# Performance work log

Measured on AMD Instinct MI355X. Metric: run time of the kernel, lower is better.

Reference implementation:

```python
import jax, jax.numpy as jnp
import numpy as np

HIDDEN = 64
NUM_LAYERS = 3
EPS = 1e-5


def setup_inputs() -> dict:
    key = jax.random.key(0)
    ks = jax.random.split(key, 16)
    N, E, F_IN, H, C = 100000, 3200000, 12, HIDDEN, 2
    x = jax.random.normal(ks[0], (N, F_IN), dtype=jnp.float32)
    edge_index = jax.random.randint(ks[1], (2, E), 0, N, dtype=jnp.int64)
    s = lambda k, sh, fan: jax.random.normal(k, sh, dtype=jnp.float32) / np.sqrt(fan)
    return {
        "x": x,
        "edge_index": edge_index,
        "W_in": s(ks[2], (F_IN, H), F_IN),
        "b_in": jnp.zeros((H,), jnp.float32),
        "W_g": s(ks[3], (NUM_LAYERS, H, H), H),
        "b_g": jnp.zeros((NUM_LAYERS, H), jnp.float32),
        "gamma": jnp.ones((NUM_LAYERS, H), jnp.float32),
        "beta": jnp.zeros((NUM_LAYERS, H), jnp.float32),
        "W_c1": s(ks[4], (H, H // 2), H),
        "b_c1": jnp.zeros((H // 2,), jnp.float32),
        "W_c2": s(ks[5], (H // 2, C), H // 2),
        "b_c2": jnp.zeros((C,), jnp.float32),
    }


def _gcn_norm(edge_index, N):
    # GCNConv default: add self loops, symmetric normalization D^-1/2 (A+I) D^-1/2
    src, dst = edge_index[0], edge_index[1]
    deg = jax.ops.segment_sum(jnp.ones_like(dst, jnp.float32), dst, num_segments=N) + 1.0
    dinv = jax.lax.rsqrt(deg)
    norm_e = dinv[src] * dinv[dst]          # [E] per-edge coefficient
    self_norm = dinv * dinv                 # [N] self-loop coefficient
    return src, dst, norm_e, self_norm


def _gcn_layer(h, W, b, src, dst, norm_e, self_norm, N):
    h = h @ W                                # [N, H] linear transform first
    agg = jax.ops.segment_sum(h[src] * norm_e[:, None], dst, num_segments=N)
    return agg + h * self_norm[:, None] + b


def _batchnorm(h, gamma, beta):
    mu = jnp.mean(h, axis=0)
    var = jnp.mean(jnp.square(h - mu), axis=0)  # biased, as torch BN
    return (h - mu) * jax.lax.rsqrt(var + EPS) * gamma + beta


def reference(x, edge_index, W_in, b_in, W_g, b_g, gamma, beta, W_c1, b_c1, W_c2, b_c2):
    N = x.shape[0]
    src, dst, norm_e, self_norm = _gcn_norm(edge_index, N)
    h = jax.nn.relu(x @ W_in + b_in)
    for i in range(NUM_LAYERS):
        h = _gcn_layer(h, W_g[i], b_g[i], src, dst, norm_e, self_norm, N)
        h = _batchnorm(h, gamma[i], beta[i])
        if i < NUM_LAYERS - 1:
            h = jax.nn.relu(h)  # dropout omitted (inference/deterministic)
    h = jax.nn.relu(h @ W_c1 + b_c1)
    return h @ W_c2 + b_c2
```

## Files before the change

### kernel.cpp

```cpp
#include <hip/hip_runtime.h>

#define EPSV 1e-5f
#define BSH 8
#define BSZ 256
#define SBR 416

__device__ inline float blo(unsigned u) { return __uint_as_float(u << 16); }
__device__ inline float bhi(unsigned u) { return __uint_as_float(u & 0xFFFF0000u); }
__device__ inline unsigned rne16(float v) {
    unsigned u = __float_as_uint(v);
    return (u + 0x7FFFu + ((u >> 16) & 1u)) >> 16;
}
__device__ inline unsigned pk(float lo, float hi) {
    return (rne16(hi) << 16) | rne16(lo);
}


__global__ __launch_bounds__(256) void k_hist(const int* __restrict__ dst,
                                              int* __restrict__ bcount, int E) {
    __shared__ int hist[1024];
    int t = threadIdx.x;
#pragma unroll
    for (int i = 0; i < 4; i++) hist[t + 256 * i] = 0;
    __syncthreads();
    int e0 = blockIdx.x * 4096;
#pragma unroll
    for (int r = 0; r < 16; r++) {
        int e = e0 + r * 256 + t;
        if (e < E) atomicAdd(&hist[dst[e] >> BSH], 1);
    }
    __syncthreads();
#pragma unroll
    for (int i = 0; i < 4; i++) {
        int bk = t + 256 * i;
        int h = hist[bk];
        if (h) atomicAdd(&bcount[bk], h);
    }
}

__global__ __launch_bounds__(256) void k_bscan(const int* __restrict__ bcount,
                                               int* __restrict__ bstart,
                                               int* __restrict__ gcur, int NB) {
    int t = threadIdx.x;
    int base = t * 4;
    int c[4], s = 0;
#pragma unroll
    for (int i = 0; i < 4; i++) {
        c[i] = (base + i < NB) ? bcount[base + i] : 0;
        s += c[i];
    }
    __shared__ int ls[256];
    ls[t] = s;
    __syncthreads();
    for (int off = 1; off < 256; off <<= 1) {
        int x = (t >= off) ? ls[t - off] : 0;
        __syncthreads();
        ls[t] += x;
        __syncthreads();
    }
    int run = (t == 0) ? 0 : ls[t - 1];
#pragma unroll
    for (int i = 0; i < 4; i++) {
        bstart[base + i] = run;
        gcur[base + i] = run;
        run += c[i];
    }
    if (t == 255) bstart[1024] = ls[255];
}

__global__ __launch_bounds__(256) void k_split(const int* __restrict__ src,
                                               const int* __restrict__ dst,
                                               int* __restrict__ gcur,
                                               unsigned* __restrict__ pairs, int E) {
    __shared__ int hist[1024];
    __shared__ int gb[1024];
    int t = threadIdx.x;
    int e0 = blockIdx.x * 4096;
    int sreg[16], dreg[16];
#pragma unroll
    for (int i = 0; i < 4; i++) hist[t + 256 * i] = 0;
    __syncthreads();
#pragma unroll
    for (int r = 0; r < 16; r++) {
        int e = e0 + r * 256 + t;
        if (e < E) {
            sreg[r] = src[e];
            dreg[r] = dst[e];
            atomicAdd(&hist[dreg[r] >> BSH], 1);
        } else {
            dreg[r] = -1;
        }
    }
    __syncthreads();
#pragma unroll
    for (int i = 0; i < 4; i++) {
        int bk = t + 256 * i;
        int h = hist[bk];
        gb[bk] = h ? atomicAdd(&gcur[bk], h) : 0;
    }
    __syncthreads();
#pragma unroll
    for (int i = 0; i < 4; i++) hist[t + 256 * i] = 0;
    __syncthreads();
#pragma unroll
    for (int r = 0; r < 16; r++) {
        if (dreg[r] >= 0) {
            int bk = dreg[r] >> BSH;
            int rk = atomicAdd(&hist[bk], 1);
            pairs[gb[bk] + rk] = ((unsigned)(dreg[r] & (BSZ - 1)) << 22) |
                                 (unsigned)sreg[r];
        }
    }
}

__global__ __launch_bounds__(256) void k_build(const unsigned* __restrict__ pairs,
                                               const int* __restrict__ bstart,
                                               int* __restrict__ rowptr,
                                               int* __restrict__ rowend,
                                               float* __restrict__ dinv,
                                               int* __restrict__ colidx, int N) {
    int bid = blockIdx.x, t = threadIdx.x;
    int n0 = bid << BSH;
    int e0 = bstart[bid], e1 = bstart[bid + 1];
    __shared__ int cnt[256];
    __shared__ int ls[256];
    __shared__ int cur[256];
    cnt[t] = 0;
    __syncthreads();
    for (int e = e0 + t; e < e1; e += 256)
        atomicAdd(&cnt[pairs[e] >> 22], 1);
    __syncthreads();
    ls[t] = cnt[t];
    __syncthreads();
    for (int off = 1; off < 256; off <<= 1) {
        int x = (t >= off) ? ls[t - off] : 0;
        __syncthreads();
        ls[t] += x;
        __syncthreads();
    }
    int start = e0 + ((t == 0) ? 0 : ls[t - 1]);
    cur[t] = start;
    int node = n0 + t;
    if (node < N) {
        rowptr[node] = start;
        rowend[node] = start + cnt[t];
        dinv[node] = rsqrtf((float)cnt[t] + 1.0f);
    }
    __syncthreads();
    for (int e = e0 + t; e < e1; e += 256) {
        unsigned p = pairs[e];
        int r = atomicAdd(&cur[p >> 22], 1);
        colidx[r] = (int)(p & 0x3FFFFFu);
    }
}


__global__ __launch_bounds__(256) void k_gemm0(const float* __restrict__ x,
                                               const float* __restrict__ Win,
                                               const float* __restrict__ bin,
                                               const float* __restrict__ W,
                                               const float* __restrict__ dinv,
                                               unsigned short* __restrict__ hl, int N) {
    __shared__ float zbuf[4][64];
    int wv = threadIdx.x >> 6;
    int j = threadIdx.x & 63;
    float w[64];
#pragma unroll
    for (int k = 0; k < 64; k++) w[k] = W[k * 64 + j];
    float wi[12];
#pragma unroll
    for (int k = 0; k < 12; k++) wi[k] = Win[k * 64 + j];
    float bj = bin[j];
    const float4* zr = (const float4*)&zbuf[wv][0];
    int wave = (blockIdx.x * 256 + threadIdx.x) >> 6;
    int nw = (gridDim.x * 256) >> 6;
    int node = wave;
    float xa[12];
    if (node < N) {
        const float* xr = x + (size_t)node * 12;
#pragma unroll
        for (int k = 0; k < 12; k++) xa[k] = xr[k];
    }
    for (; node < N; node += nw) {
        int nxt = node + nw;
        float xb[12];
        const float* xr2 = x + (size_t)(nxt < N ? nxt : node) * 12;
#pragma unroll
        for (int k = 0; k < 12; k++) xb[k] = xr2[k];
        float z = bj;
#pragma unroll
        for (int k = 0; k < 12; k++) z = fmaf(xa[k], wi[k], z);
        zbuf[wv][j] = fmaxf(z, 0.0f);
        asm volatile("s_waitcnt lgkmcnt(0)" ::: "memory");
        float acc = 0.0f;
#pragma unroll
        for (int kk = 0; kk < 16; kk++) {
            float4 z4 = zr[kk];
            acc = fmaf(z4.x, w[4 * kk + 0], acc);
            acc = fmaf(z4.y, w[4 * kk + 1], acc);
            acc = fmaf(z4.z, w[4 * kk + 2], acc);
            acc = fmaf(z4.w, w[4 * kk + 3], acc);
        }
        hl[(size_t)node * 64 + j] = (unsigned short)rne16(acc * dinv[node]);
#pragma unroll
        for (int k = 0; k < 12; k++) xa[k] = xb[k];
    }
}

__global__ __launch_bounds__(256) void k_gemmn(const float* __restrict__ W,
                                               const float* __restrict__ ab,
                                               const float* __restrict__ dinv,
                                               const unsigned* __restrict__ h2,
                                               unsigned short* __restrict__ hl, int N) {
    __shared__ float zbuf[4][64];
    int wv = threadIdx.x >> 6;
    int j = threadIdx.x & 63;
    float w[64];
#pragma unroll
    for (int k = 0; k < 64; k++) w[k] = W[k * 64 + j];
    float Aj = ab[j], Bj = ab[64 + j];
    const float4* zr = (const float4*)&zbuf[wv][0];
    int wave = (blockIdx.x * 256 + threadIdx.x) >> 6;
    int nw = (gridDim.x * 256) >> 6;
    int node = wave;
    unsigned u = (node < N) ? h2[(size_t)node * 32 + (j >> 1)] : 0u;
    for (; node < N; node += nw) {
        int nxt = node + nw;
        unsigned unext = h2[(size_t)(nxt < N ? nxt : node) * 32 + (j >> 1)];
        float h = (j & 1) ? bhi(u) : blo(u);
        zbuf[wv][j] = fmaxf(fmaf(Aj, h, Bj), 0.0f);
        asm volatile("s_waitcnt lgkmcnt(0)" ::: "memory");
        float acc = 0.0f;
#pragma unroll
        for (int kk = 0; kk < 16; kk++) {
            float4 z4 = zr[kk];
            acc = fmaf(z4.x, w[4 * kk + 0], acc);
            acc = fmaf(z4.y, w[4 * kk + 1], acc);
            acc = fmaf(z4.z, w[4 * kk + 2], acc);
            acc = fmaf(z4.w, w[4 * kk + 3], acc);
        }
        hl[(size_t)node * 64 + j] = (unsigned short)rne16(acc * dinv[node]);
        u = unext;
    }
}

__global__ __launch_bounds__(256) void k_agg(const int* __restrict__ rowptr,
                                             const int* __restrict__ rowend,
                                             const int* __restrict__ colidx,
                                             const float* __restrict__ dinv,
                                             const unsigned* __restrict__ hl2,
                                             const float* __restrict__ b,
                                             unsigned* __restrict__ out2, int N) {
    int t = threadIdx.x;
    int hw = t >> 5;
    int lane = t & 31;
    int sub = lane >> 3;
    int q = lane & 7;
    int d = blockIdx.x * 8 + hw;
    if (d >= N) return;
    int e0 = rowptr[d], e1 = rowend[d];
    const uint4* H = (const uint4*)hl2;

    float a0 = 0.f, a1 = 0.f, a2 = 0.f, a3 = 0.f;
    float a4 = 0.f, a5 = 0.f, a6 = 0.f, a7 = 0.f;
    float c0 = 0.f, c1 = 0.f, c2 = 0.f, c3 = 0.f;
    float c4 = 0.f, c5 = 0.f, c6 = 0.f, c7 = 0.f;

    if (sub == 0) {
        uint4 su = H[d * 8 + q];
        a0 = blo(su.x); a1 = bhi(su.x);
        a2 = blo(su.y); a3 = bhi(su.y);
        a4 = blo(su.z); a5 = bhi(su.z);
        a6 = blo(su.w); a7 = bhi(su.w);
    }

    int e = e0 + sub;
    for (; e + 12 < e1; e += 16) {
        int s0 = colidx[e];
        int s1 = colidx[e + 4];
        int s2 = colidx[e + 8];
        int s3 = colidx[e + 12];
        uint4 u0 = H[s0 * 8 + q];
        uint4 u1 = H[s1 * 8 + q];
        uint4 u2 = H[s2 * 8 + q];
        uint4 u3 = H[s3 * 8 + q];
        a0 += blo(u0.x); a1 += bhi(u0.x); a2 += blo(u0.y); a3 += bhi(u0.y);
        a4 += blo(u0.z); a5 += bhi(u0.z); a6 += blo(u0.w); a7 += bhi(u0.w);
        c0 += blo(u1.x); c1 += bhi(u1.x); c2 += blo(u1.y); c3 += bhi(u1.y);
        c4 += blo(u1.z); c5 += bhi(u1.z); c6 += blo(u1.w); c7 += bhi(u1.w);
        a0 += blo(u2.x); a1 += bhi(u2.x); a2 += blo(u2.y); a3 += bhi(u2.y);
        a4 += blo(u2.z); a5 += bhi(u2.z); a6 += blo(u2.w); a7 += bhi(u2.w);
        c0 += blo(u3.x); c1 += bhi(u3.x); c2 += blo(u3.y); c3 += bhi(u3.y);
        c4 += blo(u3.z); c5 += bhi(u3.z); c6 += blo(u3.w); c7 += bhi(u3.w);
    }
    for (; e < e1; e += 4) {
        uint4 u = H[colidx[e] * 8 + q];
        a0 += blo(u.x); a1 += bhi(u.x); a2 += blo(u.y); a3 += bhi(u.y);
        a4 += blo(u.z); a5 += bhi(u.z); a6 += blo(u.w); a7 += bhi(u.w);
    }
    a0 += c0; a1 += c1; a2 += c2; a3 += c3;
    a4 += c4; a5 += c5; a6 += c6; a7 += c7;

    a0 += __shfl_xor(a0, 8);  a0 += __shfl_xor(a0, 16);
    a1 += __shfl_xor(a1, 8);  a1 += __shfl_xor(a1, 16);
    a2 += __shfl_xor(a2, 8);  a2 += __shfl_xor(a2, 16);
    a3 += __shfl_xor(a3, 8);  a3 += __shfl_xor(a3, 16);
    a4 += __shfl_xor(a4, 8);  a4 += __shfl_xor(a4, 16);
    a5 += __shfl_xor(a5, 8);  a5 += __shfl_xor(a5, 16);
    a6 += __shfl_xor(a6, 8);  a6 += __shfl_xor(a6, 16);
    a7 += __shfl_xor(a7, 8);  a7 += __shfl_xor(a7, 16);

    if (sub == 0) {
        float dv = dinv[d];
        int fb = q * 8;
        float o0 = fmaf(a0, dv, b[fb + 0]);
        float o1 = fmaf(a1, dv, b[fb + 1]);
        float o2 = fmaf(a2, dv, b[fb + 2]);
        float o3 = fmaf(a3, dv, b[fb + 3]);
        float o4 = fmaf(a4, dv, b[fb + 4]);
        float o5 = fmaf(a5, dv, b[fb + 5]);
        float o6 = fmaf(a6, dv, b[fb + 6]);
        float o7 = fmaf(a7, dv, b[fb + 7]);
        uint4 o;
        o.x = pk(o0, o1);
        o.y = pk(o2, o3);
        o.z = pk(o4, o5);
        o.w = pk(o6, o7);
        ((uint4*)out2)[d * 8 + q] = o;
    }
}

__global__ __launch_bounds__(256) void k_statsred(const unsigned* __restrict__ h2,
                                                  float* __restrict__ ps,
                                                  int* __restrict__ ticket,
                                                  const float* __restrict__ gamma,
                                                  const float* __restrict__ beta,
                                                  float* __restrict__ ab,
                                                  int N, float invN) {
    int t = threadIdx.x;
    int hw = t >> 5, f = t & 31;
    float s0 = 0.f, s1 = 0.f, q0 = 0.f, q1 = 0.f;
    int stride = gridDim.x << 3;
    int n = blockIdx.x * 8 + hw;
    for (; n + 3 * stride < N; n += stride << 2) {
        unsigned ua = h2[(size_t)n * 32 + f];
        unsigned ub = h2[((size_t)n + stride) * 32 + f];
        unsigned uc = h2[((size_t)n + 2 * stride) * 32 + f];
        unsigned ud = h2[((size_t)n + 3 * stride) * 32 + f];
        float r;
        r = blo(ua); s0 += r; q0 = fmaf(r, r, q0);
        r = bhi(ua); s1 += r; q1 = fmaf(r, r, q1);
        r = blo(ub); s0 += r; q0 = fmaf(r, r, q0);
        r = bhi(ub); s1 += r; q1 = fmaf(r, r, q1);
        r = blo(uc); s0 += r; q0 = fmaf(r, r, q0);
        r = bhi(uc); s1 += r; q1 = fmaf(r, r, q1);
        r = blo(ud); s0 += r; q0 = fmaf(r, r, q0);
        r = bhi(ud); s1 += r; q1 = fmaf(r, r, q1);
    }
    for (; n < N; n += stride) {
        unsigned u = h2[(size_t)n * 32 + f];
        float r;
        r = blo(u); s0 += r; q0 = fmaf(r, r, q0);
        r = bhi(u); s1 += r; q1 = fmaf(r, r, q1);
    }
    __shared__ float rs[8][64];
    __shared__ float rq[8][64];
    __shared__ int lastflag;
    rs[hw][2 * f] = s0; rs[hw][2 * f + 1] = s1;
    rq[hw][2 * f] = q0; rq[hw][2 * f + 1] = q1;
    __syncthreads();
    if (t < 128) {
        float acc = 0.f;
#pragma unroll
        for (int h = 0; h < 8; h++) acc += (t < 64) ? rs[h][t] : rq[h][t - 64];
        atomicAdd(&ps[t], acc);
    }
    __syncthreads();
    if (t == 0) {
        __threadfence();
        lastflag = (atomicAdd(ticket, 1) == (int)gridDim.x - 1);
    }
    __syncthreads();
    if (lastflag && t < 64) {
        float S = atomicAdd(&ps[t], 0.0f);
        float Q = atomicAdd(&ps[64 + t], 0.0f);
        float mu = S * invN;
        float var = fmaf(-mu, mu, Q * invN);
        float A = rsqrtf(var + EPSV) * gamma[t];
        ab[t] = A;
        ab[64 + t] = fmaf(-mu, A, beta[t]);
    }
}

__global__ __launch_bounds__(256, 2) void k_cls(const unsigned* __restrict__ h2,
                                                const float* __restrict__ ab,
                                                const float* __restrict__ W1,
                                                const float* __restrict__ b1,
                                                const float* __restrict__ W2,
                                                const float* __restrict__ b2,
                                                float* __restrict__ out, int N) {
    int lane = threadIdx.x & 63;
    int half = lane >> 5, jj = lane & 31;
    float w[64];
    float bj = b1[jj];
#pragma unroll
    for (int k = 0; k < 64; k++) {
        float w1 = W1[k * 32 + jj];
        w[k] = ab[k] * w1;
        bj = fmaf(ab[64 + k], w1, bj);
    }
    float w20 = W2[jj * 2 + 0], w21 = W2[jj * 2 + 1];
    float b20 = b2[0], b21 = b2[1];
    int wave = (blockIdx.x * 256 + threadIdx.x) >> 6;
    int nw = (gridDim.x * 256) >> 6;
    for (int base = wave * 2; base < N; base += nw * 2) {
        int node = base + half;
        int vnode = node < N ? node : 0;
        const uint4* row = (const uint4*)(h2 + vnode * 32);
        float A0 = bj, A1 = 0.f, A2 = 0.f, A3 = 0.f;
#pragma unroll
        for (int kk = 0; kk < 8; kk++) {
            uint4 u = row[kk];
            A0 = fmaf(blo(u.x), w[8 * kk + 0], A0);
            A1 = fmaf(bhi(u.x), w[8 * kk + 1], A1);
            A2 = fmaf(blo(u.y), w[8 * kk + 2], A2);
            A3 = fmaf(bhi(u.y), w[8 * kk + 3], A3);
            A0 = fmaf(blo(u.z), w[8 * kk + 4], A0);
            A1 = fmaf(bhi(u.z), w[8 * kk + 5], A1);
            A2 = fmaf(blo(u.w), w[8 * kk + 6], A2);
            A3 = fmaf(bhi(u.w), w[8 * kk + 7], A3);
        }
        float acc = (A0 + A1) + (A2 + A3);
        float hv = fmaxf(acc, 0.0f);
        float t0 = hv * w20, t1 = hv * w21;
#pragma unroll
        for (int m = 1; m <= 16; m <<= 1) {
            t0 += __shfl_xor(t0, m, 64);
            t1 += __shfl_xor(t1, m, 64);
        }
        if (jj == 0 && node < N) {
            ((float2*)out)[node] = make_float2(t0 + b20, t1 + b21);
        }
    }
}

extern "C" void kernel_launch(void* const* d_in, const int* in_sizes, int n_in,
                              void* d_out, int out_size, void* d_ws, size_t ws_size,
                              hipStream_t stream) {
    const float* x     = (const float*)d_in[0];
    const int*   ei    = (const int*)d_in[1];
    const float* Win   = (const float*)d_in[2];
    const float* bin   = (const float*)d_in[3];
    const float* Wg    = (const float*)d_in[4];
    const float* bg    = (const float*)d_in[5];
    const float* gamma = (const float*)d_in[6];
    const float* beta  = (const float*)d_in[7];
    const float* W1    = (const float*)d_in[8];
    const float* b1    = (const float*)d_in[9];
    const float* W2    = (const float*)d_in[10];
    const float* b2    = (const float*)d_in[11];
    float* out = (float*)d_out;

    int N = in_sizes[0] / 12;
    int E = in_sizes[1] / 2;
    const int* src = ei;
    const int* dst = ei + E;
    float invN = 1.0f / (float)N;
    int NB = (N + BSZ - 1) >> BSH;

    char* ws = (char*)d_ws;
    size_t szhin = ((size_t)N * 64 * 2 + 255) / 256 * 256;
    size_t szE4  = ((size_t)E * 4 + 255) / 256 * 256;
    size_t szN4  = ((size_t)N * 4 + 255) / 256 * 256;

    size_t off = 0;
    unsigned* hin2     = (unsigned*)(ws + off); off += szhin;
    unsigned short* hl = (unsigned short*)(ws + off); off += szhin;
    int* colidx        = (int*)(ws + off); off += szE4;
    int* rowptr        = (int*)(ws + off); off += szN4;
    int* rowend        = (int*)(ws + off); off += szN4;
    float* dinv        = (float*)(ws + off); off += szN4;
    int* bcount        = (int*)(ws + off); off += 4096;
    float* ps3         = (float*)(ws + off); off += 3 * 512;
    int* tick          = (int*)(ws + off); off += 16;
    size_t msz = 4096 + 3 * 512 + 16;
    int* bstart        = (int*)(ws + off); off += 8192;
    int* gcur          = (int*)(ws + off); off += 4096;
    float* ab          = (float*)(ws + off); off += 512;

    unsigned* pairs = (unsigned*)ws;
    size_t need = off;
    if (2 * szhin < (size_t)E * 4) {
        pairs = (unsigned*)(ws + off);
        need += (size_t)E * 4;
    }
    if (ws_size < need || NB > 1024 || N >= (1 << 22)) return;

    hipMemsetAsync(bcount, 0, msz, stream);

    int EB = (E + 4095) / 4096;
    k_hist<<<EB, 256, 0, stream>>>(dst, bcount, E);
    k_bscan<<<1, 256, 0, stream>>>(bcount, bstart, gcur, NB);
    k_split<<<EB, 256, 0, stream>>>(src, dst, gcur, pairs, E);
    k_build<<<NB, 256, 0, stream>>>(pairs, bstart, rowptr, rowend, dinv, colidx, N);

    int AB = (N + 7) / 8;
    for (int i = 0; i < 3; i++) {
        if (i == 0)
            k_gemm0<<<2048, 256, 0, stream>>>(x, Win, bin, Wg, dinv, hl, N);
        else
            k_gemmn<<<2048, 256, 0, stream>>>(Wg + i * 64 * 64, ab, dinv, hin2,
                                              hl, N);
        k_agg<<<AB, 256, 0, stream>>>(rowptr, rowend, colidx, dinv,
                                      (const unsigned*)hl, bg + i * 64, hin2, N);
        k_statsred<<<SBR, 256, 0, stream>>>(hin2, ps3 + i * 128, tick + i,
                                            gamma + i * 64, beta + i * 64, ab,
                                            N, invN);
    }
    k_cls<<<1024, 256, 0, stream>>>(hin2, ab, W1, b1, W2, b2, out, N);
}
```

Before: 481.6 us.

## Switch dense GEMM kernels to thread-per-node with weights in shared memory

Rewrites k_gemm0, k_gemmn and k_cls so that each thread computes a full 64-wide (or 32-wide) output row for one node. The weights are staged in LDS and read as broadcast float4 loads, replacing the previous wave-per-node scheme that exchanged activations through LDS with an explicit wait. Outputs are packed as bf16 and written with vectorized uint4 stores, and grid sizes are reduced to 512 blocks. This is meant to cut LDS round-trips and per-node synchronization, but it raises register pressure with 64 accumulators per thread and makes per-thread global reads of each row uncoalesced.

```diff
diff --git a/kernel.cpp b/kernel.cpp
--- a/kernel.cpp
+++ b/kernel.cpp
@@ -155,55 +155,65 @@
 }
 
 
+#define GETU(hp, kk) (((kk) & 3) == 0 ? hp[(kk) >> 2].x : ((kk) & 3) == 1 ? hp[(kk) >> 2].y : ((kk) & 3) == 2 ? hp[(kk) >> 2].z : hp[(kk) >> 2].w)
+
 __global__ __launch_bounds__(256) void k_gemm0(const float* __restrict__ x,
                                                const float* __restrict__ Win,
                                                const float* __restrict__ bin,
                                                const float* __restrict__ W,
                                                const float* __restrict__ dinv,
                                                unsigned short* __restrict__ hl, int N) {
-    __shared__ float zbuf[4][64];
-    int wv = threadIdx.x >> 6;
-    int j = threadIdx.x & 63;
-    float w[64];
-#pragma unroll
-    for (int k = 0; k < 64; k++) w[k] = W[k * 64 + j];
-    float wi[12];
-#pragma unroll
-    for (int k = 0; k < 12; k++) wi[k] = Win[k * 64 + j];
-    float bj = bin[j];
-    const float4* zr = (const float4*)&zbuf[wv][0];
-    int wave = (blockIdx.x * 256 + threadIdx.x) >> 6;
-    int nw = (gridDim.x * 256) >> 6;
-    int node = wave;
-    float xa[12];
-    if (node < N) {
-        const float* xr = x + (size_t)node * 12;
-#pragma unroll
-        for (int k = 0; k < 12; k++) xa[k] = xr[k];
-    }
-    for (; node < N; node += nw) {
-        int nxt = node + nw;
-        float xb[12];
-        const float* xr2 = x + (size_t)(nxt < N ? nxt : node) * 12;
-#pragma unroll
-        for (int k = 0; k < 12; k++) xb[k] = xr2[k];
-        float z = bj;
-#pragma unroll
-        for (int k = 0; k < 12; k++) z = fmaf(xa[k], wi[k], z);
-        zbuf[wv][j] = fmaxf(z, 0.0f);
-        asm volatile("s_waitcnt lgkmcnt(0)" ::: "memory");
-        float acc = 0.0f;
-#pragma unroll
-        for (int kk = 0; kk < 16; kk++) {
-            float4 z4 = zr[kk];
-            acc = fmaf(z4.x, w[4 * kk + 0], acc);
-            acc = fmaf(z4.y, w[4 * kk + 1], acc);
-            acc = fmaf(z4.z, w[4 * kk + 2], acc);
-            acc = fmaf(z4.w, w[4 * kk + 3], acc);
-        }
-        hl[(size_t)node * 64 + j] = (unsigned short)rne16(acc * dinv[node]);
-#pragma unroll
-        for (int k = 0; k < 12; k++) xa[k] = xb[k];
+    __shared__ float WL[4096];
+    __shared__ float WT[64][16];
+    int t = threadIdx.x;
+    for (int i = t; i < 4096; i += 256) WL[i] = W[i];
+    for (int i = t; i < 1024; i += 256) {
+        int k = i >> 4, m = i & 15;
+        WT[k][m] = (m < 12) ? Win[m * 64 + k] : (m == 12 ? bin[k] : 0.0f);
+    }
+    __syncthreads();
+    const float4* WL4 = (const float4*)WL;
+    const float4* WT4 = (const float4*)&WT[0][0];
+    for (int node = blockIdx.x * 256 + t; node < N; node += gridDim.x * 256) {
+        const float4* xrw = (const float4*)(x + (size_t)node * 12);
+        float4 xa = xrw[0], xb = xrw[1], xc = xrw[2];
+        float acc[64];
+#pragma unroll
+        for (int f = 0; f < 64; f++) acc[f] = 0.0f;
+#pragma unroll
+        for (int k = 0; k < 64; k++) {
+            float4 wa = WT4[k * 4 + 0];
+            float4 wb = WT4[k * 4 + 1];
+            float4 wc = WT4[k * 4 + 2];
+            float4 wd = WT4[k * 4 + 3];
+            float z = wd.x;
+            z = fmaf(xa.x, wa.x, z); z = fmaf(xa.y, wa.y, z);
+            z = fmaf(xa.z, wa.z, z); z = fmaf(xa.w, wa.w, z);
+            z = fmaf(xb.x, wb.x, z); z = fmaf(xb.y, wb.y, z);
+            z = fmaf(xb.z, wb.z, z); z = fmaf(xb.w, wb.w, z);
+            z = fmaf(xc.x, wc.x, z); z = fmaf(xc.y, wc.y, z);
+            z = fmaf(xc.z, wc.z, z); z = fmaf(xc.w, wc.w, z);
+            z = fmaxf(z, 0.0f);
+#pragma unroll
+            for (int f = 0; f < 16; f++) {
+                float4 w4 = WL4[k * 16 + f];
+                acc[4 * f + 0] = fmaf(z, w4.x, acc[4 * f + 0]);
+                acc[4 * f + 1] = fmaf(z, w4.y, acc[4 * f + 1]);
+                acc[4 * f + 2] = fmaf(z, w4.z, acc[4 * f + 2]);
+                acc[4 * f + 3] = fmaf(z, w4.w, acc[4 * f + 3]);
+            }
+        }
+        float dv = dinv[node];
+        uint4* orow = (uint4*)(hl + (size_t)node * 64);
+#pragma unroll
+        for (int i = 0; i < 8; i++) {
+            uint4 o;
+            o.x = pk(acc[8 * i + 0] * dv, acc[8 * i + 1] * dv);
+            o.y = pk(acc[8 * i + 2] * dv, acc[8 * i + 3] * dv);
+            o.z = pk(acc[8 * i + 4] * dv, acc[8 * i + 5] * dv);
+            o.w = pk(acc[8 * i + 6] * dv, acc[8 * i + 7] * dv);
+            orow[i] = o;
+        }
     }
 }
 
@@ -212,35 +222,52 @@
                                                const float* __restrict__ dinv,
                                                const unsigned* __restrict__ h2,
                                                unsigned short* __restrict__ hl, int N) {
-    __shared__ float zbuf[4][64];
-    int wv = threadIdx.x >> 6;
-    int j = threadIdx.x & 63;
-    float w[64];
-#pragma unroll
-    for (int k = 0; k < 64; k++) w[k] = W[k * 64 + j];
-    float Aj = ab[j], Bj = ab[64 + j];
-    const float4* zr = (const float4*)&zbuf[wv][0];
-    int wave = (blockIdx.x * 256 + threadIdx.x) >> 6;
-    int nw = (gridDim.x * 256) >> 6;
-    int node = wave;
-    unsigned u = (node < N) ? h2[(size_t)node * 32 + (j >> 1)] : 0u;
-    for (; node < N; node += nw) {
-        int nxt = node + nw;
-        unsigned unext = h2[(size_t)(nxt < N ? nxt : node) * 32 + (j >> 1)];
-        float h = (j & 1) ? bhi(u) : blo(u);
-        zbuf[wv][j] = fmaxf(fmaf(Aj, h, Bj), 0.0f);
-        asm volatile("s_waitcnt lgkmcnt(0)" ::: "memory");
-        float acc = 0.0f;
-#pragma unroll
-        for (int kk = 0; kk < 16; kk++) {
-            float4 z4 = zr[kk];
-            acc = fmaf(z4.x, w[4 * kk + 0], acc);
-            acc = fmaf(z4.y, w[4 * kk + 1], acc);
-            acc = fmaf(z4.z, w[4 * kk + 2], acc);
-            acc = fmaf(z4.w, w[4 * kk + 3], acc);
-        }
-        hl[(size_t)node * 64 + j] = (unsigned short)rne16(acc * dinv[node]);
-        u = unext;
+    __shared__ float WL[4096];
+    __shared__ float ABL[256];
+    int t = threadIdx.x;
+    for (int i = t; i < 4096; i += 256) WL[i] = W[i];
+    if (t < 64) {
+        ABL[4 * (t >> 1) + 2 * (t & 1) + 0] = ab[t];
+        ABL[4 * (t >> 1) + 2 * (t & 1) + 1] = ab[64 + t];
+    }
+    __syncthreads();
+    const float4* WL4 = (const float4*)WL;
+    const float4* AB4 = (const float4*)ABL;
+    for (int node = blockIdx.x * 256 + t; node < N; node += gridDim.x * 256) {
+        const uint4* hr = (const uint4*)(h2 + (size_t)node * 32);
+        uint4 hp[8];
+#pragma unroll
+        for (int i = 0; i < 8; i++) hp[i] = hr[i];
+        float acc[64];
+#pragma unroll
+        for (int f = 0; f < 64; f++) acc[f] = 0.0f;
+#pragma unroll
+        for (int kk = 0; kk < 32; kk++) {
+            unsigned u = GETU(hp, kk);
+            float4 abv = AB4[kk];
+            float z0 = fmaxf(fmaf(abv.x, blo(u), abv.y), 0.0f);
+            float z1 = fmaxf(fmaf(abv.z, bhi(u), abv.w), 0.0f);
+#pragma unroll
+            for (int f = 0; f < 16; f++) {
+                float4 w0 = WL4[(2 * kk) * 16 + f];
+                float4 w1 = WL4[(2 * kk + 1) * 16 + f];
+                acc[4 * f + 0] = fmaf(z1, w1.x, fmaf(z0, w0.x, acc[4 * f + 0]));
+                acc[4 * f + 1] = fmaf(z1, w1.y, fmaf(z0, w0.y, acc[4 * f + 1]));
+                acc[4 * f + 2] = fmaf(z1, w1.z, fmaf(z0, w0.z, acc[4 * f + 2]));
+                acc[4 * f + 3] = fmaf(z1, w1.w, fmaf(z0, w0.w, acc[4 * f + 3]));
+            }
+        }
+        float dv = dinv[node];
+        uint4* orow = (uint4*)(hl + (size_t)node * 64);
+#pragma unroll
+        for (int i = 0; i < 8; i++) {
+            uint4 o;
+            o.x = pk(acc[8 * i + 0] * dv, acc[8 * i + 1] * dv);
+            o.y = pk(acc[8 * i + 2] * dv, acc[8 * i + 3] * dv);
+            o.z = pk(acc[8 * i + 4] * dv, acc[8 * i + 5] * dv);
+            o.w = pk(acc[8 * i + 6] * dv, acc[8 * i + 7] * dv);
+            orow[i] = o;
+        }
     }
 }
 
@@ -392,55 +419,64 @@
     }
 }
 
-__global__ __launch_bounds__(256, 2) void k_cls(const unsigned* __restrict__ h2,
-                                                const float* __restrict__ ab,
-                                                const float* __restrict__ W1,
-                                                const float* __restrict__ b1,
-                                                const float* __restrict__ W2,
-                                                const float* __restrict__ b2,
-                                                float* __restrict__ out, int N) {
-    int lane = threadIdx.x & 63;
-    int half = lane >> 5, jj = lane & 31;
-    float w[64];
-    float bj = b1[jj];
-#pragma unroll
-    for (int k = 0; k < 64; k++) {
-        float w1 = W1[k * 32 + jj];
-        w[k] = ab[k] * w1;
-        bj = fmaf(ab[64 + k], w1, bj);
-    }
-    float w20 = W2[jj * 2 + 0], w21 = W2[jj * 2 + 1];
+__global__ __launch_bounds__(256) void k_cls(const unsigned* __restrict__ h2,
+                                             const float* __restrict__ ab,
+                                             const float* __restrict__ W1,
+                                             const float* __restrict__ b1,
+                                             const float* __restrict__ W2,
+                                             const float* __restrict__ b2,
+                                             float* __restrict__ out, int N) {
+    __shared__ float W1L[2048];
+    __shared__ float b1L[32];
+    __shared__ float W2L[64];
+    int t = threadIdx.x;
+    for (int i = t; i < 2048; i += 256) W1L[i] = ab[i >> 5] * W1[i];
+    if (t < 64) W2L[t] = W2[t];
+    if (t < 32) {
+        float s = b1[t];
+        for (int k = 0; k < 64; k++) s = fmaf(ab[64 + k], W1[k * 32 + t], s);
+        b1L[t] = s;
+    }
+    __syncthreads();
+    const float4* W1L4 = (const float4*)W1L;
+    const float4* b1L4 = (const float4*)b1L;
+    const float2* W2L2 = (const float2*)W2L;
     float b20 = b2[0], b21 = b2[1];
-    int wave = (blockIdx.x * 256 + threadIdx.x) >> 6;
-    int nw = (gridDim.x * 256) >> 6;
-    for (int base = wave * 2; base < N; base += nw * 2) {
-        int node = base + half;
-        int vnode = node < N ? node : 0;
-        const uint4* row = (const uint4*)(h2 + vnode * 32);
-        float A0 = bj, A1 = 0.f, A2 = 0.f, A3 = 0.f;
-#pragma unroll
-        for (int kk = 0; kk < 8; kk++) {
-            uint4 u = row[kk];
-            A0 = fmaf(blo(u.x), w[8 * kk + 0], A0);
-            A1 = fmaf(bhi(u.x), w[8 * kk + 1], A1);
-            A2 = fmaf(blo(u.y), w[8 * kk + 2], A2);
-            A3 = fmaf(bhi(u.y), w[8 * kk + 3], A3);
-            A0 = fmaf(blo(u.z), w[8 * kk + 4], A0);
-            A1 = fmaf(bhi(u.z), w[8 * kk + 5], A1);
-            A2 = fmaf(blo(u.w), w[8 * kk + 6], A2);
-            A3 = fmaf(bhi(u.w), w[8 * kk + 7], A3);
-        }
-        float acc = (A0 + A1) + (A2 + A3);
-        float hv = fmaxf(acc, 0.0f);
-        float t0 = hv * w20, t1 = hv * w21;
-#pragma unroll
-        for (int m = 1; m <= 16; m <<= 1) {
-            t0 += __shfl_xor(t0, m, 64);
-            t1 += __shfl_xor(t1, m, 64);
-        }
-        if (jj == 0 && node < N) {
-            ((float2*)out)[node] = make_float2(t0 + b20, t1 + b21);
-        }
+    for (int node = blockIdx.x * 256 + t; node < N; node += gridDim.x * 256) {
+        const uint4* hr = (const uint4*)(h2 + (size_t)node * 32);
+        uint4 hp[8];
+#pragma unroll
+        for (int i = 0; i < 8; i++) hp[i] = hr[i];
+        float acc[32];
+#pragma unroll
+        for (int jj4 = 0; jj4 < 8; jj4++) {
+            float4 bb = b1L4[jj4];
+            acc[4 * jj4 + 0] = bb.x; acc[4 * jj4 + 1] = bb.y;
+            acc[4 * jj4 + 2] = bb.z; acc[4 * jj4 + 3] = bb.w;
+        }
+#pragma unroll
+        for (int kk = 0; kk < 32; kk++) {
+            unsigned u = GETU(hp, kk);
+            float z0 = blo(u), z1 = bhi(u);
+#pragma unroll
+            for (int f = 0; f < 8; f++) {
+                float4 w0 = W1L4[(2 * kk) * 8 + f];
+                float4 w1 = W1L4[(2 * kk + 1) * 8 + f];
+                acc[4 * f + 0] = fmaf(z1, w1.x, fmaf(z0, w0.x, acc[4 * f + 0]));
+                acc[4 * f + 1] = fmaf(z1, w1.y, fmaf(z0, w0.y, acc[4 * f + 1]));
+                acc[4 * f + 2] = fmaf(z1, w1.z, fmaf(z0, w0.z, acc[4 * f + 2]));
+                acc[4 * f + 3] = fmaf(z1, w1.w, fmaf(z0, w0.w, acc[4 * f + 3]));
+            }
+        }
+        float o0 = b20, o1 = b21;
+#pragma unroll
+        for (int jj = 0; jj < 32; jj++) {
+            float hv = fmaxf(acc[jj], 0.0f);
+            float2 w2 = W2L2[jj];
+            o0 = fmaf(hv, w2.x, o0);
+            o1 = fmaf(hv, w2.y, o1);
+        }
+        ((float2*)out)[node] = make_float2(o0, o1);
     }
 }
 
@@ -507,15 +543,15 @@
     int AB = (N + 7) / 8;
     for (int i = 0; i < 3; i++) {
         if (i == 0)
-            k_gemm0<<<2048, 256, 0, stream>>>(x, Win, bin, Wg, dinv, hl, N);
+            k_gemm0<<<512, 256, 0, stream>>>(x, Win, bin, Wg, dinv, hl, N);
         else
-            k_gemmn<<<2048, 256, 0, stream>>>(Wg + i * 64 * 64, ab, dinv, hin2,
-                                              hl, N);
+            k_gemmn<<<512, 256, 0, stream>>>(Wg + i * 64 * 64, ab, dinv, hin2,
+                                             hl, N);
         k_agg<<<AB, 256, 0, stream>>>(rowptr, rowend, colidx, dinv,
                                       (const unsigned*)hl, bg + i * 64, hin2, N);
         k_statsred<<<SBR, 256, 0, stream>>>(hin2, ps3 + i * 128, tick + i,
                                             gamma + i * 64, beta + i * 64, ab,
                                             N, invN);
     }
-    k_cls<<<1024, 256, 0, stream>>>(hin2, ab, W1, b1, W2, b2, out, N);
-}
+    k_cls<<<512, 256, 0, stream>>>(hin2, ab, W1, b1, W2, b2, out, N);
+}
```

Result: slower. 815.1 us (+69.3%).

## Replace global atomic bucket cursors with per-block histogram matrix and column scan

Applied to the files above, without the earlier changes.

Per-block bucket histograms are written to a block-by-bucket matrix instead of being atomically accumulated. A new multi-block kernel exclusive-scans each bucket column across blocks, and the last block to finish scans the bucket totals. The split pass then reads precomputed offsets, so it no longer recounts its histogram or does atomics on global cursors. This removes the contended global atomics and one histogram pass, at the cost of writing and reading a histogram matrix of about 3 MB plus a strided column scan.

```diff
diff --git a/kernel.cpp b/kernel.cpp
--- a/kernel.cpp
+++ b/kernel.cpp
@@ -17,7 +17,7 @@
 
 
 __global__ __launch_bounds__(256) void k_hist(const int* __restrict__ dst,
-                                              int* __restrict__ bcount, int E) {
+                                              int* __restrict__ histmat, int E) {
     __shared__ int hist[1024];
     int t = threadIdx.x;
 #pragma unroll
@@ -30,77 +30,94 @@
         if (e < E) atomicAdd(&hist[dst[e] >> BSH], 1);
     }
     __syncthreads();
-#pragma unroll
-    for (int i = 0; i < 4; i++) {
-        int bk = t + 256 * i;
-        int h = hist[bk];
-        if (h) atomicAdd(&bcount[bk], h);
-    }
-}
-
-__global__ __launch_bounds__(256) void k_bscan(const int* __restrict__ bcount,
+    int* hrow = histmat + (size_t)blockIdx.x * 1024;
+#pragma unroll
+    for (int i = 0; i < 4; i++) hrow[t + 256 * i] = hist[t + 256 * i];
+}
+
+__global__ __launch_bounds__(256) void k_scanb(int* __restrict__ histmat,
+                                               int* __restrict__ bcount,
                                                int* __restrict__ bstart,
-                                               int* __restrict__ gcur, int NB) {
+                                               int* __restrict__ ticket,
+                                               int NBLK) {
     int t = threadIdx.x;
-    int base = t * 4;
-    int c[4], s = 0;
-#pragma unroll
-    for (int i = 0; i < 4; i++) {
-        c[i] = (base + i < NB) ? bcount[base + i] : 0;
-        s += c[i];
-    }
-    __shared__ int ls[256];
-    ls[t] = s;
-    __syncthreads();
-    for (int off = 1; off < 256; off <<= 1) {
-        int x = (t >= off) ? ls[t - off] : 0;
+    int wv = t >> 6, lane = t & 63;
+    int bucket = blockIdx.x * 4 + wv;
+    int run = 0;
+    int lim = (NBLK + 63) & ~63;
+    for (int i = lane; i < lim; i += 64) {
+        int v = (i < NBLK) ? histmat[(size_t)i * 1024 + bucket] : 0;
+        int s = v;
+#pragma unroll
+        for (int d = 1; d < 64; d <<= 1) {
+            int up = __shfl_up(s, d, 64);
+            if (lane >= d) s += up;
+        }
+        if (i < NBLK) histmat[(size_t)i * 1024 + bucket] = run + s - v;
+        run += __shfl(s, 63, 64);
+    }
+    if (lane == 0) bcount[bucket] = run;
+    __syncthreads();
+    __shared__ int lastflag;
+    if (t == 0) {
+        __threadfence();
+        lastflag = (atomicAdd(ticket, 1) == (int)gridDim.x - 1);
+    }
+    __syncthreads();
+    if (lastflag) {
+        int base = t * 4;
+        int c[4], s2 = 0;
+#pragma unroll
+        for (int i = 0; i < 4; i++) {
+            c[i] = atomicAdd(&bcount[base + i], 0);
+            s2 += c[i];
+        }
+        __shared__ int ls[256];
+        ls[t] = s2;
         __syncthreads();
-        ls[t] += x;
-        __syncthreads();
-    }
-    int run = (t == 0) ? 0 : ls[t - 1];
-#pragma unroll
-    for (int i = 0; i < 4; i++) {
-        bstart[base + i] = run;
-        gcur[base + i] = run;
-        run += c[i];
-    }
-    if (t == 255) bstart[1024] = ls[255];
+        for (int off = 1; off < 256; off <<= 1) {
+            int x = (t >= off) ? ls[t - off] : 0;
+            __syncthreads();
+            ls[t] += x;
+            __syncthreads();
+        }
+        int run2 = (t == 0) ? 0 : ls[t - 1];
+#pragma unroll
+        for (int i = 0; i < 4; i++) {
+            bstart[base + i] = run2;
+            run2 += c[i];
+        }
+        if (t == 255) bstart[1024] = ls[255];
+    }
 }
 
 __global__ __launch_bounds__(256) void k_split(const int* __restrict__ src,
                                                const int* __restrict__ dst,
-                                               int* __restrict__ gcur,
+                                               const int* __restrict__ histmat,
+                                               const int* __restrict__ bstart,
                                                unsigned* __restrict__ pairs, int E) {
     __shared__ int hist[1024];
     __shared__ int gb[1024];
     int t = threadIdx.x;
     int e0 = blockIdx.x * 4096;
+    const int* hrow = histmat + (size_t)blockIdx.x * 1024;
     int sreg[16], dreg[16];
 #pragma unroll
-    for (int i = 0; i < 4; i++) hist[t + 256 * i] = 0;
-    __syncthreads();
+    for (int i = 0; i < 4; i++) {
+        int bk = t + 256 * i;
+        hist[bk] = 0;
+        gb[bk] = bstart[bk] + hrow[bk];
+    }
 #pragma unroll
     for (int r = 0; r < 16; r++) {
         int e = e0 + r * 256 + t;
         if (e < E) {
             sreg[r] = src[e];
             dreg[r] = dst[e];
-            atomicAdd(&hist[dreg[r] >> BSH], 1);
         } else {
             dreg[r] = -1;
         }
     }
-    __syncthreads();
-#pragma unroll
-    for (int i = 0; i < 4; i++) {
-        int bk = t + 256 * i;
-        int h = hist[bk];
-        gb[bk] = h ? atomicAdd(&gcur[bk], h) : 0;
-    }
-    __syncthreads();
-#pragma unroll
-    for (int i = 0; i < 4; i++) hist[t + 256 * i] = 0;
     __syncthreads();
 #pragma unroll
     for (int r = 0; r < 16; r++) {
@@ -467,6 +484,7 @@
     const int* dst = ei + E;
     float invN = 1.0f / (float)N;
     int NB = (N + BSZ - 1) >> BSH;
+    int NBLK = (E + 4095) / 4096;
 
     char* ws = (char*)d_ws;
     size_t szhin = ((size_t)N * 64 * 2 + 255) / 256 * 256;
@@ -482,26 +500,27 @@
     float* dinv        = (float*)(ws + off); off += szN4;
     int* bcount        = (int*)(ws + off); off += 4096;
     float* ps3         = (float*)(ws + off); off += 3 * 512;
-    int* tick          = (int*)(ws + off); off += 16;
-    size_t msz = 4096 + 3 * 512 + 16;
+    int* tick          = (int*)(ws + off); off += 32;
+    size_t msz = 4096 + 3 * 512 + 32;
     int* bstart        = (int*)(ws + off); off += 8192;
-    int* gcur          = (int*)(ws + off); off += 4096;
     float* ab          = (float*)(ws + off); off += 512;
 
     unsigned* pairs = (unsigned*)ws;
+    int* histmat = (int*)(ws + szhin);
     size_t need = off;
-    if (2 * szhin < (size_t)E * 4) {
+    if ((size_t)E * 4 > szhin || (size_t)NBLK * 4096 > szhin) {
         pairs = (unsigned*)(ws + off);
-        need += (size_t)E * 4;
-    }
-    if (ws_size < need || NB > 1024 || N >= (1 << 22)) return;
+        histmat = (int*)(ws + off + szE4);
+        need = off + szE4 + (size_t)NBLK * 4096;
+    }
+    if (ws_size < need || NB > 1024 || N >= (1 << 22) || NBLK > 3072)
+        return;
 
     hipMemsetAsync(bcount, 0, msz, stream);
 
-    int EB = (E + 4095) / 4096;
-    k_hist<<<EB, 256, 0, stream>>>(dst, bcount, E);
-    k_bscan<<<1, 256, 0, stream>>>(bcount, bstart, gcur, NB);
-    k_split<<<EB, 256, 0, stream>>>(src, dst, gcur, pairs, E);
+    k_hist<<<NBLK, 256, 0, stream>>>(dst, histmat, E);
+    k_scanb<<<256, 256, 0, stream>>>(histmat, bcount, bstart, tick + 3, NBLK);
+    k_split<<<NBLK, 256, 0, stream>>>(src, dst, histmat, bstart, pairs, E);
     k_build<<<NB, 256, 0, stream>>>(pairs, bstart, rowptr, rowend, dinv, colidx, N);
 
     int AB = (N + 7) / 8;
```

Result: faster. 467.7 us (-2.9%).
